# Performance work log

Measured on AMD Instinct MI355X. Metric: run time of the kernel, lower is better.

## Reference

```python
import jax, jax.numpy as jnp
import numpy as np

N, E, F_IN, H, MH, C, G = 100000, 3200000, 128, 32, 64, 10, 64

def _seg_sum(data, ids, num):
    return jax.ops.segment_sum(data, ids, num_segments=num)

def gcn_conv(x, row, col, ew, W, b, n):
    # PyG GCNConv: linear first, then self-loops + symmetric edge-weight norm + scatter-add
    h = x @ W  # [N, H]
    loop = jnp.arange(n)
    r = jnp.concatenate([row, loop])
    c = jnp.concatenate([col, loop])
    w = jnp.concatenate([ew, jnp.ones((n,), dtype=ew.dtype)])
    deg = _seg_sum(w, c, n)
    dinv = jnp.where(deg > 0, jax.lax.rsqrt(deg), 0.0)
    norm = dinv[r] * w * dinv[c]  # [E+N]
    out = _seg_sum(norm[:, None] * h[r], c, n)  # scatter to targets
    return out + b

def setup_inputs():
    key = jax.random.key(0)
    ks = jax.random.split(key, 16)
    inp = {
        "x": jax.random.normal(ks[0], (N, F_IN), dtype=jnp.float32),
        "edge_index": jax.random.randint(ks[1], (2, E), 0, N, dtype=jnp.int64),
        "edge_weight": jax.random.uniform(ks[2], (E,), dtype=jnp.float32),
        "batch": jnp.sort(jax.random.randint(ks[3], (N,), 0, G, dtype=jnp.int64)),
    }
    def lin(k, i, o):
        s = 1.0 / np.sqrt(i)
        k1, k2 = jax.random.split(k)
        return (jax.random.uniform(k1, (i, o), minval=-s, maxval=s, dtype=jnp.float32),
                jax.random.uniform(k2, (o,), minval=-s, maxval=s, dtype=jnp.float32))
    inp["W1"], inp["b1"] = lin(ks[4], F_IN, H)
    inp["W2"], inp["b2"] = lin(ks[5], H, H)
    inp["W3"], inp["b3"] = lin(ks[6], H, H)
    inp["Wm0"], inp["bm0"] = lin(ks[7], H, MH)
    inp["Wm1"], inp["bm1"] = lin(ks[8], MH, MH)
    inp["Wout"], inp["bout"] = lin(ks[9], MH, C)
    return inp

def reference(x, edge_index, edge_weight, batch, W1, b1, W2, b2, W3, b3, Wm0, bm0, Wm1, bm1, Wout, bout):
    row, col = edge_index[0], edge_index[1]
    h = jax.nn.relu(gcn_conv(x, row, col, edge_weight, W1, b1, N))
    h = jax.nn.relu(gcn_conv(h, row, col, edge_weight, W2, b2, N))
    h = gcn_conv(h, row, col, edge_weight, W3, b3, N)
    # global mean pool over graphs
    sums = _seg_sum(h, batch, G)
    counts = _seg_sum(jnp.ones((N,), dtype=h.dtype), batch, G)
    g = sums / jnp.maximum(counts, 1.0)[:, None]
    # dropout p=0.5 is identity at inference (training=False)
    g = jax.nn.relu(g @ Wm0 + bm0)
    g = jax.nn.relu(g @ Wm1 + bm1)
    return g @ Wout + bout
```

## Files before the change

kernel.cpp:

```cpp
#include <hip/hip_runtime.h>

#define NN 100000
#define NE 3200000
#define FIN 128
#define HID 32
#define MH  64
#define NC  10
#define NG  64
#define NBKT 782
#define NBLK 512
#define EPB  (NE / NBLK)
#define SCANL (NBKT * NBLK)
#define SRCMASK 0x1FFFF
#define BCAP 5120

typedef float floatx2 __attribute__((ext_vector_type(2)));

__global__ __launch_bounds__(1024)
void hist_bkt(const int* __restrict__ ei, int* __restrict__ cnt2) {
    __shared__ int h[NBKT];
    int tid = threadIdx.x, blk = blockIdx.x;
    for (int b = tid; b < NBKT; b += 1024) h[b] = 0;
    __syncthreads();
    int base = blk * EPB;
    for (int i = tid; i < EPB; i += 1024)
        atomicAdd(&h[ei[NE + base + i] >> 7], 1);
    __syncthreads();
    for (int b = tid; b < NBKT; b += 1024) cnt2[b * NBLK + blk] = h[b];
}

__global__ void scan_block(const int* __restrict__ in, int* __restrict__ out,
                           int* __restrict__ bsum, int n) {
    __shared__ int lds[256];
    int tid = threadIdx.x;
    int base = blockIdx.x * 1024 + tid * 4;
    int v0 = 0, v1 = 0, v2 = 0, v3 = 0;
    if (base + 0 < n) v0 = in[base + 0];
    if (base + 1 < n) v1 = in[base + 1];
    if (base + 2 < n) v2 = in[base + 2];
    if (base + 3 < n) v3 = in[base + 3];
    int s = v0 + v1 + v2 + v3;
    lds[tid] = s;
    __syncthreads();
    for (int off = 1; off < 256; off <<= 1) {
        int val = (tid >= off) ? lds[tid - off] : 0;
        __syncthreads();
        lds[tid] += val;
        __syncthreads();
    }
    int excl = lds[tid] - s;
    if (tid == 255) bsum[blockIdx.x] = lds[255];
    if (base + 0 < n) out[base + 0] = excl;
    if (base + 1 < n) out[base + 1] = excl + v0;
    if (base + 2 < n) out[base + 2] = excl + v0 + v1;
    if (base + 3 < n) out[base + 3] = excl + v0 + v1 + v2;
}

__global__ void scan_top(int* __restrict__ bsum, int nb, float* __restrict__ sc) {
    int lane = threadIdx.x;
    for (int i = lane; i < NG * HID + NG; i += 64) sc[i] = 0.0f;
    int carry = 0;
    for (int base = 0; base < nb; base += 64) {
        int i = base + lane;
        int orig = (i < nb) ? bsum[i] : 0;
        int v = orig;
#pragma unroll
        for (int off = 1; off < 64; off <<= 1) {
            int t = __shfl_up(v, off, 64);
            if (lane >= off) v += t;
        }
        if (i < nb) bsum[i] = carry + v - orig;
        carry += __shfl(v, 63, 64);
    }
}

__global__ void scan_add(int* __restrict__ data, const int* __restrict__ bsum, int n) {
    int i = blockIdx.x * 256 + threadIdx.x;
    if (i < n) data[i] += bsum[i >> 10];
}

__global__ __launch_bounds__(1024)
void scatter_bkt(const int* __restrict__ ei, const float* __restrict__ ew,
                 const int* __restrict__ cnt2, const int* __restrict__ scanned,
                 int2* __restrict__ tre) {
    __shared__ int2 pay[EPB];
    __shared__ int scur[NBKT];
    __shared__ int hexc[NBKT];
    __shared__ int gbase[NBKT];
    int tid = threadIdx.x, blk = blockIdx.x;
    int myh = 0;
    if (tid < NBKT) {
        myh = cnt2[tid * NBLK + blk];
        gbase[tid] = scanned[tid * NBLK + blk];
        scur[tid] = myh;
    }
    __syncthreads();
    for (int off = 1; off < NBKT; off <<= 1) {
        int v = (tid < NBKT && tid >= off) ? scur[tid - off] : 0;
        __syncthreads();
        if (tid < NBKT) scur[tid] += v;
        __syncthreads();
    }
    if (tid < NBKT) { int ex = scur[tid] - myh; hexc[tid] = ex; scur[tid] = ex; }
    __syncthreads();
    int base = blk * EPB;
    for (int i = tid; i < EPB; i += 1024) {
        int e = base + i;
        int c = ei[NE + e];
        int r = ei[e];
        unsigned int wb = __float_as_uint(ew[e]);
        int b = c >> 7;
        int j = atomicAdd(&scur[b], 1);
        pay[j] = make_int2(r | ((c & 127) << 17) | ((b & 0xFF) << 24),
                           (int)((wb & ~3u) | ((unsigned)b >> 8)));
    }
    __syncthreads();
    for (int j = tid; j < EPB; j += 1024) {
        int2 q = pay[j];
        int b = (int)((((unsigned)q.y & 3u) << 8) | (((unsigned)q.x >> 24) & 0xFFu));
        int pos = gbase[b] + (j - hexc[b]);
        tre[pos] = make_int2(q.x & 0x00FFFFFF, q.y & ~3);
    }
}

__global__ __launch_bounds__(512)
void sort_k(const int2* __restrict__ tre, const int* __restrict__ scanned,
            unsigned int* __restrict__ srn4, int* __restrict__ rowptr,
            float* __restrict__ dinv) {
    __shared__ int2 ed[BCAP];
    __shared__ int h[128];
    __shared__ float dw[128];
    __shared__ int cur[128];
    int b = blockIdx.x, tid = threadIdx.x;
    int base = scanned[b * NBLK];
    int end = (b == NBKT - 1) ? NE : scanned[(b + 1) * NBLK];
    int n = end - base;
    bool staged = (n <= BCAP);
    if (tid < 128) { h[tid] = 0; dw[tid] = 0.f; }
    __syncthreads();
    for (int i = tid; i < n; i += 512) {
        int2 q = tre[base + i];
        if (staged) ed[i] = q;
        int key = (q.x >> 17) & 127;
        atomicAdd(&h[key], 1);
        atomicAdd(&dw[key], __int_as_float(q.y));
    }
    __syncthreads();
    if (tid < 64) {
        int lane = tid;
        int carry = 0;
#pragma unroll
        for (int c = 0; c < 2; ++c) {
            int idx = c * 64 + lane;
            int hv = h[idx];
            int v = hv;
#pragma unroll
            for (int off = 1; off < 64; off <<= 1) {
                int t = __shfl_up(v, off, 64);
                if (lane >= off) v += t;
            }
            cur[idx] = base + carry + v - hv;
            int node = b * 128 + idx;
            if (node < NN) {
                rowptr[node] = base + carry + v;
                dinv[node] = rsqrtf(1.0f + dw[idx]);
            }
            carry += __shfl(v, 63, 64);
        }
    }
    __syncthreads();
    for (int i = tid; i < n; i += 512) {
        int2 q = staged ? ed[i] : tre[base + i];
        int key = (q.x >> 17) & 127;
        int pos = atomicAdd(&cur[key], 1);
        unsigned int wb = (unsigned)q.y;
        wb += 0x7FFFu + ((wb >> 16) & 1u);
        srn4[pos] = (unsigned)(q.x & SRCMASK) | (((wb >> 16) & 0x7FFFu) << 17);
    }
}

template <int IN_DIM, bool RELU_IN>
__global__ __launch_bounds__(256)
void linear_k(const float* __restrict__ in, const float* __restrict__ W,
              const float* __restrict__ dinv, unsigned int* __restrict__ tmp8) {
    constexpr int J4 = IN_DIM / 4;
    constexpr int XSS = J4 + 1;
    __shared__ float4 xs[64 * XSS];
    __shared__ float4 wp[IN_DIM * 8];
    int tid = threadIdx.x;
    for (int idx = tid; idx < IN_DIM * 8; idx += 256) {
        int j = idx >> 3, kg = idx & 7;
        const float* wr = W + j * 32 + kg * 4;
        wp[idx] = make_float4(wr[0], wr[1], wr[2], wr[3]);
    }
    int rbase = blockIdx.x * 64;
    const float4* in4 = (const float4*)in;
    for (int idx = tid; idx < 64 * J4; idx += 256) {
        int row = idx / J4, j4 = idx % J4;
        int grow = rbase + row;
        float4 v = (grow < NN) ? in4[(size_t)grow * J4 + j4]
                               : make_float4(0.f, 0.f, 0.f, 0.f);
        if (RELU_IN) {
            v.x = fmaxf(v.x, 0.f); v.y = fmaxf(v.y, 0.f);
            v.z = fmaxf(v.z, 0.f); v.w = fmaxf(v.w, 0.f);
        }
        xs[row * XSS + j4] = v;
    }
    __syncthreads();
    int kg = tid & 7;
    int rp = tid >> 3;
    int r0 = rbase + 2 * rp;
    if (r0 >= NN) return;
    const float4* x0 = &xs[(2 * rp) * XSS];
    const float4* x1 = &xs[(2 * rp + 1) * XSS];
    float a00 = 0, a01 = 0, a02 = 0, a03 = 0;
    float a10 = 0, a11 = 0, a12 = 0, a13 = 0;
#pragma unroll
    for (int j4 = 0; j4 < J4; ++j4) {
        float4 v0 = x0[j4], v1 = x1[j4];
        const float4* wj = &wp[j4 * 4 * 8 + kg];
        float4 w0 = wj[0], w1 = wj[8], w2 = wj[16], w3 = wj[24];
#define LSTEP(VX0, VX1, W4) \
        a00 = fmaf(VX0, W4.x, a00); a01 = fmaf(VX0, W4.y, a01); \
        a02 = fmaf(VX0, W4.z, a02); a03 = fmaf(VX0, W4.w, a03); \
        a10 = fmaf(VX1, W4.x, a10); a11 = fmaf(VX1, W4.y, a11); \
        a12 = fmaf(VX1, W4.z, a12); a13 = fmaf(VX1, W4.w, a13);
        LSTEP(v0.x, v1.x, w0)
        LSTEP(v0.y, v1.y, w1)
        LSTEP(v0.z, v1.z, w2)
        LSTEP(v0.w, v1.w, w3)
#undef LSTEP
    }
    float d0 = dinv[r0], d1 = dinv[r0 + 1];
    a00 *= d0; a01 *= d0; a02 *= d0; a03 *= d0;
    a10 *= d1; a11 *= d1; a12 *= d1; a13 *= d1;
    int q0 = __builtin_amdgcn_cvt_pk_fp8_f32(a00, a01, 0, false);
    q0 = __builtin_amdgcn_cvt_pk_fp8_f32(a02, a03, q0, true);
    int q1 = __builtin_amdgcn_cvt_pk_fp8_f32(a10, a11, 0, false);
    q1 = __builtin_amdgcn_cvt_pk_fp8_f32(a12, a13, q1, true);
    tmp8[r0 * 8 + kg] = (unsigned int)q0;
    tmp8[(r0 + 1) * 8 + kg] = (unsigned int)q1;
}

__device__ __forceinline__ float4 agg_core(const unsigned int* __restrict__ srn4,
                                           const int* __restrict__ rowptr,
                                           const unsigned int* __restrict__ tmp8,
                                           int wid, int g, int q) {
    unsigned int qb = (unsigned int)q * 4u;
    const char* t8 = (const char*)tmp8;
    int end = rowptr[wid];
    int start = (wid == 0) ? 0 : rowptr[wid - 1];
    floatx2 a01 = {0.f, 0.f}, a23 = {0.f, 0.f};
    floatx2 c01 = {0.f, 0.f}, c23 = {0.f, 0.f};
    int e = start + g;
    for (; e + 24 < end; e += 32) {
        unsigned int p0 = srn4[e];
        unsigned int p1 = srn4[e + 8];
        unsigned int p2 = srn4[e + 16];
        unsigned int p3 = srn4[e + 24];
        unsigned int u0 = *(const unsigned int*)(t8 + (((p0 & SRCMASK) << 5) | qb));
        unsigned int u1 = *(const unsigned int*)(t8 + (((p1 & SRCMASK) << 5) | qb));
        unsigned int u2 = *(const unsigned int*)(t8 + (((p2 & SRCMASK) << 5) | qb));
        unsigned int u3 = *(const unsigned int*)(t8 + (((p3 & SRCMASK) << 5) | qb));
        float w0 = __uint_as_float((p0 >> 1) & 0x7FFF0000u);
        float w1 = __uint_as_float((p1 >> 1) & 0x7FFF0000u);
        float w2 = __uint_as_float((p2 >> 1) & 0x7FFF0000u);
        float w3 = __uint_as_float((p3 >> 1) & 0x7FFF0000u);
        floatx2 lo, hi;
        lo = __builtin_amdgcn_cvt_pk_f32_fp8(u0, false);
        hi = __builtin_amdgcn_cvt_pk_f32_fp8(u0, true);
        a01 += lo * w0; a23 += hi * w0;
        lo = __builtin_amdgcn_cvt_pk_f32_fp8(u1, false);
        hi = __builtin_amdgcn_cvt_pk_f32_fp8(u1, true);
        c01 += lo * w1; c23 += hi * w1;
        lo = __builtin_amdgcn_cvt_pk_f32_fp8(u2, false);
        hi = __builtin_amdgcn_cvt_pk_f32_fp8(u2, true);
        a01 += lo * w2; a23 += hi * w2;
        lo = __builtin_amdgcn_cvt_pk_f32_fp8(u3, false);
        hi = __builtin_amdgcn_cvt_pk_f32_fp8(u3, true);
        c01 += lo * w3; c23 += hi * w3;
    }
    for (; e < end; e += 8) {
        unsigned int p = srn4[e];
        unsigned int u = *(const unsigned int*)(t8 + (((p & SRCMASK) << 5) | qb));
        float w = __uint_as_float((p >> 1) & 0x7FFF0000u);
        floatx2 lo = __builtin_amdgcn_cvt_pk_f32_fp8(u, false);
        floatx2 hi = __builtin_amdgcn_cvt_pk_f32_fp8(u, true);
        a01 += lo * w; a23 += hi * w;
    }
    a01 += c01; a23 += c23;
    float a0 = a01.x, a1 = a01.y, a2 = a23.x, a3 = a23.y;
    a0 += __shfl_xor(a0, 8, 64);  a1 += __shfl_xor(a1, 8, 64);
    a2 += __shfl_xor(a2, 8, 64);  a3 += __shfl_xor(a3, 8, 64);
    a0 += __shfl_xor(a0, 16, 64); a1 += __shfl_xor(a1, 16, 64);
    a2 += __shfl_xor(a2, 16, 64); a3 += __shfl_xor(a3, 16, 64);
    a0 += __shfl_xor(a0, 32, 64); a1 += __shfl_xor(a1, 32, 64);
    a2 += __shfl_xor(a2, 32, 64); a3 += __shfl_xor(a3, 32, 64);
    return make_float4(a0, a1, a2, a3);
}

__global__ __launch_bounds__(256)
void aggregate(const unsigned int* __restrict__ srn4,
               const int* __restrict__ rowptr,
               const float* __restrict__ dinv,
               const float* __restrict__ bias,
               const unsigned int* __restrict__ tmp8,
               float* __restrict__ h) {
    int tid = threadIdx.x;
    int wid = (blockIdx.x * 256 + tid) >> 6;
    if (wid >= NN) return;
    int lane = tid & 63;
    int g = lane >> 3, q = lane & 7;
    float4 a = agg_core(srn4, rowptr, tmp8, wid, g, q);
    if (g == 0) {
        float d = dinv[wid];
        unsigned int sv = tmp8[(size_t)wid * 8 + q];
        floatx2 slo = __builtin_amdgcn_cvt_pk_f32_fp8(sv, false);
        floatx2 shi = __builtin_amdgcn_cvt_pk_f32_fp8(sv, true);
        float4 bq = ((const float4*)bias)[q];
        float4 o;
        o.x = bq.x + d * (slo.x + a.x);
        o.y = bq.y + d * (slo.y + a.y);
        o.z = bq.z + d * (shi.x + a.z);
        o.w = bq.w + d * (shi.y + a.w);
        ((float4*)(h + (size_t)wid * HID))[q] = o;
    }
}

__global__ __launch_bounds__(256)
void agg_lin(const unsigned int* __restrict__ srn4,
             const int* __restrict__ rowptr,
             const float* __restrict__ dinv,
             const float* __restrict__ bias,
             const float* __restrict__ Wn,
             const unsigned int* __restrict__ tmp8,
             unsigned int* __restrict__ tmp8_out) {
    __shared__ float hrow[4][HID];
    int tid = threadIdx.x;
    int wid = (blockIdx.x * 256 + tid) >> 6;
    int wv = tid >> 6;
    int lane = tid & 63;
    int g = lane >> 3, q = lane & 7;
    float4 a = agg_core(srn4, rowptr, tmp8, wid, g, q);
    float d = dinv[wid];
    if (g == 0) {
        unsigned int sv = tmp8[(size_t)wid * 8 + q];
        floatx2 slo = __builtin_amdgcn_cvt_pk_f32_fp8(sv, false);
        floatx2 shi = __builtin_amdgcn_cvt_pk_f32_fp8(sv, true);
        float4 bq = ((const float4*)bias)[q];
        float4 o;
        o.x = fmaxf(bq.x + d * (slo.x + a.x), 0.f);
        o.y = fmaxf(bq.y + d * (slo.y + a.y), 0.f);
        o.z = fmaxf(bq.z + d * (shi.x + a.z), 0.f);
        o.w = fmaxf(bq.w + d * (shi.y + a.w), 0.f);
        *((float4*)&hrow[wv][4 * q]) = o;
    }
    int j = lane & 31, half = lane >> 5;
    const float4* h4 = (const float4*)&hrow[wv][half * 16];
    float4 h0 = h4[0], h1 = h4[1], h2 = h4[2], h3 = h4[3];
    float hh[16];
    *((float4*)&hh[0]) = h0; *((float4*)&hh[4]) = h1;
    *((float4*)&hh[8]) = h2; *((float4*)&hh[12]) = h3;
    const float* wc = Wn + half * 16 * 32 + j;
    float y = 0.f;
#pragma unroll
    for (int k = 0; k < 16; ++k)
        y = fmaf(hh[k], wc[k * 32], y);
    y += __shfl_xor(y, 32, 64);
    y *= d;
    float y1 = __shfl_down(y, 1, 64);
    float y2 = __shfl_down(y, 2, 64);
    float y3 = __shfl_down(y, 3, 64);
    if (half == 0 && (j & 3) == 0) {
        int w0 = __builtin_amdgcn_cvt_pk_fp8_f32(y, y1, 0, false);
        w0 = __builtin_amdgcn_cvt_pk_fp8_f32(y2, y3, w0, true);
        tmp8_out[wid * 8 + (j >> 2)] = (unsigned int)w0;
    }
}

__global__ void pool_k(const float* __restrict__ h, const int* __restrict__ batch,
                       float* __restrict__ sums, float* __restrict__ counts) {
    int t = blockIdx.x * 256 + threadIdx.x;
    int chunk = t >> 5, k = t & 31;
    int n0 = chunk * 32;
    if (n0 >= NN) return;
    int n1 = min(n0 + 32, NN);
    int g = batch[n0];
    float acc = 0.f, cacc = 0.f;
    for (int i = n0; i < n1; ++i) {
        int gi = batch[i];
        if (gi != g) {
            atomicAdd(&sums[g * HID + k], acc);
            if (k == 0) atomicAdd(&counts[g], cacc);
            g = gi; acc = 0.f; cacc = 0.f;
        }
        acc += h[(size_t)i * HID + k];
        cacc += 1.f;
    }
    atomicAdd(&sums[g * HID + k], acc);
    if (k == 0) atomicAdd(&counts[g], cacc);
}

__global__ __launch_bounds__(64)
void mlp_k(const float* __restrict__ sums, const float* __restrict__ counts,
           const float* __restrict__ Wm0, const float* __restrict__ bm0,
           const float* __restrict__ Wm1, const float* __restrict__ bm1,
           const float* __restrict__ Wout, const float* __restrict__ bout,
           float* __restrict__ out) {
    __shared__ float g0[HID];
    __shared__ float g1[MH];
    __shared__ float g2[MH];
    int g = blockIdx.x;
    int k = threadIdx.x;
    if (k < HID) g0[k] = sums[g * HID + k] / fmaxf(counts[g], 1.0f);
    __syncthreads();
    float acc = bm0[k];
#pragma unroll
    for (int j = 0; j < HID; ++j) acc = fmaf(g0[j], Wm0[j * MH + k], acc);
    g1[k] = fmaxf(acc, 0.f);
    __syncthreads();
    float acc2 = bm1[k];
#pragma unroll
    for (int j = 0; j < MH; ++j) acc2 = fmaf(g1[j], Wm1[j * MH + k], acc2);
    g2[k] = fmaxf(acc2, 0.f);
    __syncthreads();
    if (k < NC) {
        float acc3 = bout[k];
#pragma unroll
        for (int j = 0; j < MH; ++j) acc3 = fmaf(g2[j], Wout[j * NC + k], acc3);
        out[g * NC + k] = acc3;
    }
}

extern "C" void kernel_launch(void* const* d_in, const int* in_sizes, int n_in,
                              void* d_out, int out_size, void* d_ws, size_t ws_size,
                              hipStream_t stream) {
    const float* x    = (const float*)d_in[0];
    const int*   ei   = (const int*)d_in[1];
    const float* ew   = (const float*)d_in[2];
    const int*   batch= (const int*)d_in[3];
    const float* W1   = (const float*)d_in[4];
    const float* b1   = (const float*)d_in[5];
    const float* W2   = (const float*)d_in[6];
    const float* b2   = (const float*)d_in[7];
    const float* W3   = (const float*)d_in[8];
    const float* b3   = (const float*)d_in[9];
    const float* Wm0  = (const float*)d_in[10];
    const float* bm0  = (const float*)d_in[11];
    const float* Wm1  = (const float*)d_in[12];
    const float* bm1  = (const float*)d_in[13];
    const float* Wout = (const float*)d_in[14];
    const float* bout = (const float*)d_in[15];
    float* out = (float*)d_out;

    char* p = (char*)d_ws;
    unsigned int* srn4 = (unsigned int*)p; p += sizeof(unsigned int) * (size_t)NE;
    char*  S   = p;                      p += 12 * (size_t)NE;
    int2*  tre = (int2*)S;
    int*   cnt2    = (int*)(S + sizeof(int2) * (size_t)NE);
    int*   scanned = cnt2 + SCANL;
    unsigned int* tmp8  = (unsigned int*)S;
    unsigned int* tmp8b = tmp8 + (size_t)NN * 8;
    float* hA  = (float*)(S + 2 * (size_t)NN * HID);
    int*   bsum    = (int*)p;            p += sizeof(int) * 512;
    float* dinv    = (float*)p;          p += sizeof(float) * NN;
    int*   rowptr  = (int*)p;            p += sizeof(int) * NN;
    float* sums    = (float*)p;          p += sizeof(float) * NG * HID;
    float* counts  = (float*)p;

    dim3 blk(256);
    const int NB_SCAN = (SCANL + 1023) / 1024;
    const int NB_LIN = (NN + 63) / 64;

    hist_bkt<<<NBLK, 1024, 0, stream>>>(ei, cnt2);
    scan_block<<<NB_SCAN, blk, 0, stream>>>(cnt2, scanned, bsum, SCANL);
    scan_top<<<1, 64, 0, stream>>>(bsum, NB_SCAN, sums);
    scan_add<<<(SCANL + 255) / 256, blk, 0, stream>>>(scanned, bsum, SCANL);
    scatter_bkt<<<NBLK, 1024, 0, stream>>>(ei, ew, cnt2, scanned, tre);
    sort_k<<<NBKT, 512, 0, stream>>>(tre, scanned, srn4, rowptr, dinv);

    linear_k<FIN, false><<<NB_LIN, blk, 0, stream>>>(x, W1, dinv, tmp8);
    agg_lin<<<25000, blk, 0, stream>>>(srn4, rowptr, dinv, b1, W2, tmp8, tmp8b);
    agg_lin<<<25000, blk, 0, stream>>>(srn4, rowptr, dinv, b2, W3, tmp8b, tmp8);
    aggregate<<<25000, blk, 0, stream>>>(srn4, rowptr, dinv, b3, tmp8, hA);

    pool_k<<<391, blk, 0, stream>>>(hA, batch, sums, counts);
    mlp_k<<<NG, 64, 0, stream>>>(sums, counts, Wm0, bm0, Wm1, bm1, Wout, bout, out);
}
```

Measured before the change: 398.8 us.

## Aggregate one node per half-wavefront with 8-byte fp8 gathers per lane

The three aggregation kernels now give each node 32 lanes instead of a full 64-lane wavefront. Each lane loads 8 fp8 features (uint2) instead of 4, and 8 edge slots are processed in parallel. The cross-lane reduction shrinks to three shuffle stages, and the fused linear step in agg_lin runs a full 32-wide dot product per lane with no half-split shuffle, which halves the grid. The aim is to raise useful lanes per gather and cut reduction and launch overhead. The cost is more registers per lane and more accumulator work per thread.

Result: faster. 370.7 us (-7.0%).

```diff
diff --git a/kernel.cpp b/kernel.cpp
--- a/kernel.cpp
+++ b/kernel.cpp
@@ -242,61 +242,78 @@
     tmp8[(r0 + 1) * 8 + kg] = (unsigned int)q1;
 }
 
-__device__ __forceinline__ float4 agg_core(const unsigned int* __restrict__ srn4,
-                                           const int* __restrict__ rowptr,
-                                           const unsigned int* __restrict__ tmp8,
-                                           int wid, int g, int q) {
-    unsigned int qb = (unsigned int)q * 4u;
+struct AccR { floatx2 r0, r1, r2, r3; };
+
+__device__ __forceinline__ AccR agg_core(const unsigned int* __restrict__ srn4,
+                                         const int* __restrict__ rowptr,
+                                         const unsigned int* __restrict__ tmp8,
+                                         int nid, int s, unsigned int cb) {
     const char* t8 = (const char*)tmp8;
-    int end = rowptr[wid];
-    int start = (wid == 0) ? 0 : rowptr[wid - 1];
-    floatx2 a01 = {0.f, 0.f}, a23 = {0.f, 0.f};
-    floatx2 c01 = {0.f, 0.f}, c23 = {0.f, 0.f};
-    int e = start + g;
+    int end = rowptr[nid];
+    int start = (nid == 0) ? 0 : rowptr[nid - 1];
+    floatx2 a0 = {0.f, 0.f}, a1 = {0.f, 0.f}, a2 = {0.f, 0.f}, a3 = {0.f, 0.f};
+    floatx2 b0 = {0.f, 0.f}, b1 = {0.f, 0.f}, b2 = {0.f, 0.f}, b3 = {0.f, 0.f};
+    int e = start + s;
     for (; e + 24 < end; e += 32) {
         unsigned int p0 = srn4[e];
         unsigned int p1 = srn4[e + 8];
         unsigned int p2 = srn4[e + 16];
         unsigned int p3 = srn4[e + 24];
-        unsigned int u0 = *(const unsigned int*)(t8 + (((p0 & SRCMASK) << 5) | qb));
-        unsigned int u1 = *(const unsigned int*)(t8 + (((p1 & SRCMASK) << 5) | qb));
-        unsigned int u2 = *(const unsigned int*)(t8 + (((p2 & SRCMASK) << 5) | qb));
-        unsigned int u3 = *(const unsigned int*)(t8 + (((p3 & SRCMASK) << 5) | qb));
+        uint2 u0 = *(const uint2*)(t8 + (((p0 & SRCMASK) << 5) | cb));
+        uint2 u1 = *(const uint2*)(t8 + (((p1 & SRCMASK) << 5) | cb));
+        uint2 u2 = *(const uint2*)(t8 + (((p2 & SRCMASK) << 5) | cb));
+        uint2 u3 = *(const uint2*)(t8 + (((p3 & SRCMASK) << 5) | cb));
         float w0 = __uint_as_float((p0 >> 1) & 0x7FFF0000u);
         float w1 = __uint_as_float((p1 >> 1) & 0x7FFF0000u);
         float w2 = __uint_as_float((p2 >> 1) & 0x7FFF0000u);
         float w3 = __uint_as_float((p3 >> 1) & 0x7FFF0000u);
         floatx2 lo, hi;
-        lo = __builtin_amdgcn_cvt_pk_f32_fp8(u0, false);
-        hi = __builtin_amdgcn_cvt_pk_f32_fp8(u0, true);
-        a01 += lo * w0; a23 += hi * w0;
-        lo = __builtin_amdgcn_cvt_pk_f32_fp8(u1, false);
-        hi = __builtin_amdgcn_cvt_pk_f32_fp8(u1, true);
-        c01 += lo * w1; c23 += hi * w1;
-        lo = __builtin_amdgcn_cvt_pk_f32_fp8(u2, false);
-        hi = __builtin_amdgcn_cvt_pk_f32_fp8(u2, true);
-        a01 += lo * w2; a23 += hi * w2;
-        lo = __builtin_amdgcn_cvt_pk_f32_fp8(u3, false);
-        hi = __builtin_amdgcn_cvt_pk_f32_fp8(u3, true);
-        c01 += lo * w3; c23 += hi * w3;
+        lo = __builtin_amdgcn_cvt_pk_f32_fp8(u0.x, false);
+        hi = __builtin_amdgcn_cvt_pk_f32_fp8(u0.x, true);
+        a0 += lo * w0; a1 += hi * w0;
+        lo = __builtin_amdgcn_cvt_pk_f32_fp8(u0.y, false);
+        hi = __builtin_amdgcn_cvt_pk_f32_fp8(u0.y, true);
+        a2 += lo * w0; a3 += hi * w0;
+        lo = __builtin_amdgcn_cvt_pk_f32_fp8(u1.x, false);
+        hi = __builtin_amdgcn_cvt_pk_f32_fp8(u1.x, true);
+        b0 += lo * w1; b1 += hi * w1;
+        lo = __builtin_amdgcn_cvt_pk_f32_fp8(u1.y, false);
+        hi = __builtin_amdgcn_cvt_pk_f32_fp8(u1.y, true);
+        b2 += lo * w1; b3 += hi * w1;
+        lo = __builtin_amdgcn_cvt_pk_f32_fp8(u2.x, false);
+        hi = __builtin_amdgcn_cvt_pk_f32_fp8(u2.x, true);
+        a0 += lo * w2; a1 += hi * w2;
+        lo = __builtin_amdgcn_cvt_pk_f32_fp8(u2.y, false);
+        hi = __builtin_amdgcn_cvt_pk_f32_fp8(u2.y, true);
+        a2 += lo * w2; a3 += hi * w2;
+        lo = __builtin_amdgcn_cvt_pk_f32_fp8(u3.x, false);
+        hi = __builtin_amdgcn_cvt_pk_f32_fp8(u3.x, true);
+        b0 += lo * w3; b1 += hi * w3;
+        lo = __builtin_amdgcn_cvt_pk_f32_fp8(u3.y, false);
+        hi = __builtin_amdgcn_cvt_pk_f32_fp8(u3.y, true);
+        b2 += lo * w3; b3 += hi * w3;
     }
     for (; e < end; e += 8) {
         unsigned int p = srn4[e];
-        unsigned int u = *(const unsigned int*)(t8 + (((p & SRCMASK) << 5) | qb));
+        uint2 u = *(const uint2*)(t8 + (((p & SRCMASK) << 5) | cb));
         float w = __uint_as_float((p >> 1) & 0x7FFF0000u);
-        floatx2 lo = __builtin_amdgcn_cvt_pk_f32_fp8(u, false);
-        floatx2 hi = __builtin_amdgcn_cvt_pk_f32_fp8(u, true);
-        a01 += lo * w; a23 += hi * w;
-    }
-    a01 += c01; a23 += c23;
-    float a0 = a01.x, a1 = a01.y, a2 = a23.x, a3 = a23.y;
-    a0 += __shfl_xor(a0, 8, 64);  a1 += __shfl_xor(a1, 8, 64);
-    a2 += __shfl_xor(a2, 8, 64);  a3 += __shfl_xor(a3, 8, 64);
-    a0 += __shfl_xor(a0, 16, 64); a1 += __shfl_xor(a1, 16, 64);
-    a2 += __shfl_xor(a2, 16, 64); a3 += __shfl_xor(a3, 16, 64);
-    a0 += __shfl_xor(a0, 32, 64); a1 += __shfl_xor(a1, 32, 64);
-    a2 += __shfl_xor(a2, 32, 64); a3 += __shfl_xor(a3, 32, 64);
-    return make_float4(a0, a1, a2, a3);
+        floatx2 lo = __builtin_amdgcn_cvt_pk_f32_fp8(u.x, false);
+        floatx2 hi = __builtin_amdgcn_cvt_pk_f32_fp8(u.x, true);
+        a0 += lo * w; a1 += hi * w;
+        lo = __builtin_amdgcn_cvt_pk_f32_fp8(u.y, false);
+        hi = __builtin_amdgcn_cvt_pk_f32_fp8(u.y, true);
+        a2 += lo * w; a3 += hi * w;
+    }
+    a0 += b0; a1 += b1; a2 += b2; a3 += b3;
+#pragma unroll
+    for (int m = 4; m <= 16; m <<= 1) {
+        a0.x += __shfl_xor(a0.x, m, 64); a0.y += __shfl_xor(a0.y, m, 64);
+        a1.x += __shfl_xor(a1.x, m, 64); a1.y += __shfl_xor(a1.y, m, 64);
+        a2.x += __shfl_xor(a2.x, m, 64); a2.y += __shfl_xor(a2.y, m, 64);
+        a3.x += __shfl_xor(a3.x, m, 64); a3.y += __shfl_xor(a3.y, m, 64);
+    }
+    AccR r; r.r0 = a0; r.r1 = a1; r.r2 = a2; r.r3 = a3;
+    return r;
 }
 
 __global__ __launch_bounds__(256)
@@ -307,23 +324,33 @@
                const unsigned int* __restrict__ tmp8,
                float* __restrict__ h) {
     int tid = threadIdx.x;
-    int wid = (blockIdx.x * 256 + tid) >> 6;
-    if (wid >= NN) return;
-    int lane = tid & 63;
-    int g = lane >> 3, q = lane & 7;
-    float4 a = agg_core(srn4, rowptr, tmp8, wid, g, q);
-    if (g == 0) {
-        float d = dinv[wid];
-        unsigned int sv = tmp8[(size_t)wid * 8 + q];
-        floatx2 slo = __builtin_amdgcn_cvt_pk_f32_fp8(sv, false);
-        floatx2 shi = __builtin_amdgcn_cvt_pk_f32_fp8(sv, true);
-        float4 bq = ((const float4*)bias)[q];
-        float4 o;
-        o.x = bq.x + d * (slo.x + a.x);
-        o.y = bq.y + d * (slo.y + a.y);
-        o.z = bq.z + d * (shi.x + a.z);
-        o.w = bq.w + d * (shi.y + a.w);
-        ((float4*)(h + (size_t)wid * HID))[q] = o;
+    int nid = (blockIdx.x * 256 + tid) >> 5;
+    int hl = tid & 31;
+    int c = hl & 3, s = hl >> 2;
+    unsigned int cb = (unsigned int)c * 8u;
+    AccR A = agg_core(srn4, rowptr, tmp8, nid, s, cb);
+    if (hl < 4) {
+        float d = dinv[nid];
+        const char* t8 = (const char*)tmp8;
+        uint2 sv = *(const uint2*)(t8 + ((unsigned int)nid << 5) + cb);
+        floatx2 s0 = __builtin_amdgcn_cvt_pk_f32_fp8(sv.x, false);
+        floatx2 s1 = __builtin_amdgcn_cvt_pk_f32_fp8(sv.x, true);
+        floatx2 s2 = __builtin_amdgcn_cvt_pk_f32_fp8(sv.y, false);
+        floatx2 s3 = __builtin_amdgcn_cvt_pk_f32_fp8(sv.y, true);
+        const float4* b4 = (const float4*)bias;
+        float4 bq0 = b4[2 * c], bq1 = b4[2 * c + 1];
+        float4 o0, o1;
+        o0.x = bq0.x + d * (s0.x + A.r0.x);
+        o0.y = bq0.y + d * (s0.y + A.r0.y);
+        o0.z = bq0.z + d * (s1.x + A.r1.x);
+        o0.w = bq0.w + d * (s1.y + A.r1.y);
+        o1.x = bq1.x + d * (s2.x + A.r2.x);
+        o1.y = bq1.y + d * (s2.y + A.r2.y);
+        o1.z = bq1.z + d * (s3.x + A.r3.x);
+        o1.w = bq1.w + d * (s3.y + A.r3.y);
+        float4* hp = (float4*)(h + (size_t)nid * HID);
+        hp[2 * c] = o0;
+        hp[2 * c + 1] = o1;
     }
 }
 
@@ -335,46 +362,61 @@
              const float* __restrict__ Wn,
              const unsigned int* __restrict__ tmp8,
              unsigned int* __restrict__ tmp8_out) {
-    __shared__ float hrow[4][HID];
+    __shared__ float hrow[4][2][HID];
     int tid = threadIdx.x;
-    int wid = (blockIdx.x * 256 + tid) >> 6;
+    int nid = (blockIdx.x * 256 + tid) >> 5;
     int wv = tid >> 6;
-    int lane = tid & 63;
-    int g = lane >> 3, q = lane & 7;
-    float4 a = agg_core(srn4, rowptr, tmp8, wid, g, q);
-    float d = dinv[wid];
-    if (g == 0) {
-        unsigned int sv = tmp8[(size_t)wid * 8 + q];
-        floatx2 slo = __builtin_amdgcn_cvt_pk_f32_fp8(sv, false);
-        floatx2 shi = __builtin_amdgcn_cvt_pk_f32_fp8(sv, true);
-        float4 bq = ((const float4*)bias)[q];
-        float4 o;
-        o.x = fmaxf(bq.x + d * (slo.x + a.x), 0.f);
-        o.y = fmaxf(bq.y + d * (slo.y + a.y), 0.f);
-        o.z = fmaxf(bq.z + d * (shi.x + a.z), 0.f);
-        o.w = fmaxf(bq.w + d * (shi.y + a.w), 0.f);
-        *((float4*)&hrow[wv][4 * q]) = o;
-    }
-    int j = lane & 31, half = lane >> 5;
-    const float4* h4 = (const float4*)&hrow[wv][half * 16];
+    int half = (tid >> 5) & 1;
+    int hl = tid & 31;
+    int c = hl & 3, s = hl >> 2;
+    unsigned int cb = (unsigned int)c * 8u;
+    AccR A = agg_core(srn4, rowptr, tmp8, nid, s, cb);
+    float d = dinv[nid];
+    if (hl < 4) {
+        const char* t8 = (const char*)tmp8;
+        uint2 sv = *(const uint2*)(t8 + ((unsigned int)nid << 5) + cb);
+        floatx2 s0 = __builtin_amdgcn_cvt_pk_f32_fp8(sv.x, false);
+        floatx2 s1 = __builtin_amdgcn_cvt_pk_f32_fp8(sv.x, true);
+        floatx2 s2 = __builtin_amdgcn_cvt_pk_f32_fp8(sv.y, false);
+        floatx2 s3 = __builtin_amdgcn_cvt_pk_f32_fp8(sv.y, true);
+        const float4* b4 = (const float4*)bias;
+        float4 bq0 = b4[2 * c], bq1 = b4[2 * c + 1];
+        float4 o0, o1;
+        o0.x = fmaxf(bq0.x + d * (s0.x + A.r0.x), 0.f);
+        o0.y = fmaxf(bq0.y + d * (s0.y + A.r0.y), 0.f);
+        o0.z = fmaxf(bq0.z + d * (s1.x + A.r1.x), 0.f);
+        o0.w = fmaxf(bq0.w + d * (s1.y + A.r1.y), 0.f);
+        o1.x = fmaxf(bq1.x + d * (s2.x + A.r2.x), 0.f);
+        o1.y = fmaxf(bq1.y + d * (s2.y + A.r2.y), 0.f);
+        o1.z = fmaxf(bq1.z + d * (s3.x + A.r3.x), 0.f);
+        o1.w = fmaxf(bq1.w + d * (s3.y + A.r3.y), 0.f);
+        float4* hp = (float4*)&hrow[wv][half][0];
+        hp[2 * c] = o0;
+        hp[2 * c + 1] = o1;
+    }
+    int j = hl;
+    const float* hr = hrow[wv][half];
+    const float4* h4 = (const float4*)hr;
     float4 h0 = h4[0], h1 = h4[1], h2 = h4[2], h3 = h4[3];
-    float hh[16];
-    *((float4*)&hh[0]) = h0; *((float4*)&hh[4]) = h1;
-    *((float4*)&hh[8]) = h2; *((float4*)&hh[12]) = h3;
-    const float* wc = Wn + half * 16 * 32 + j;
+    float4 h4v = h4[4], h5 = h4[5], h6 = h4[6], h7 = h4[7];
+    float hh[32];
+    *((float4*)&hh[0]) = h0;  *((float4*)&hh[4]) = h1;
+    *((float4*)&hh[8]) = h2;  *((float4*)&hh[12]) = h3;
+    *((float4*)&hh[16]) = h4v; *((float4*)&hh[20]) = h5;
+    *((float4*)&hh[24]) = h6;  *((float4*)&hh[28]) = h7;
+    const float* wc = Wn + j;
     float y = 0.f;
 #pragma unroll
-    for (int k = 0; k < 16; ++k)
+    for (int k = 0; k < 32; ++k)
         y = fmaf(hh[k], wc[k * 32], y);
-    y += __shfl_xor(y, 32, 64);
     y *= d;
     float y1 = __shfl_down(y, 1, 64);
     float y2 = __shfl_down(y, 2, 64);
     float y3 = __shfl_down(y, 3, 64);
-    if (half == 0 && (j & 3) == 0) {
+    if ((hl & 3) == 0) {
         int w0 = __builtin_amdgcn_cvt_pk_fp8_f32(y, y1, 0, false);
         w0 = __builtin_amdgcn_cvt_pk_fp8_f32(y2, y3, w0, true);
-        tmp8_out[wid * 8 + (j >> 2)] = (unsigned int)w0;
+        tmp8_out[nid * 8 + (hl >> 2)] = (unsigned int)w0;
     }
 }
 
@@ -471,6 +513,7 @@
     dim3 blk(256);
     const int NB_SCAN = (SCANL + 1023) / 1024;
     const int NB_LIN = (NN + 63) / 64;
+    const int NB_AGG = 12500;
 
     hist_bkt<<<NBLK, 1024, 0, stream>>>(ei, cnt2);
     scan_block<<<NB_SCAN, blk, 0, stream>>>(cnt2, scanned, bsum, SCANL);
@@ -480,9 +523,9 @@
     sort_k<<<NBKT, 512, 0, stream>>>(tre, scanned, srn4, rowptr, dinv);
 
     linear_k<FIN, false><<<NB_LIN, blk, 0, stream>>>(x, W1, dinv, tmp8);
-    agg_lin<<<25000, blk, 0, stream>>>(srn4, rowptr, dinv, b1, W2, tmp8, tmp8b);
-    agg_lin<<<25000, blk, 0, stream>>>(srn4, rowptr, dinv, b2, W3, tmp8b, tmp8);
-    aggregate<<<25000, blk, 0, stream>>>(srn4, rowptr, dinv, b3, tmp8, hA);
+    agg_lin<<<NB_AGG, blk, 0, stream>>>(srn4, rowptr, dinv, b1, W2, tmp8, tmp8b);
+    agg_lin<<<NB_AGG, blk, 0, stream>>>(srn4, rowptr, dinv, b2, W3, tmp8b, tmp8);
+    aggregate<<<NB_AGG, blk, 0, stream>>>(srn4, rowptr, dinv, b3, tmp8, hA);
 
     pool_k<<<391, blk, 0, stream>>>(hA, batch, sums, counts);
     mlp_k<<<NG, 64, 0, stream>>>(sums, counts, Wm0, bm0, Wm1, bm1, Wout, bout, out);
```

## Aggregate four nodes per wavefront with 16-byte fp8 gathers per lane

Applied to the files above, without the earlier changes.

Changes the aggregation kernels to map 16 lanes per destination node instead of 64. Each lane handles 16 fp8 features through a uint4 gather, so 8 edge slots times 2 column halves cover a node's 32 features. In agg_lin, the next-layer weight matrix is staged transposed in shared memory, and the matrix-vector product is done per node by 16 lanes. The intent is fewer, wider gather loads and less shuffle-reduction overhead per node, at the cost of more registers for accumulators and more load imbalance within a wavefront across nodes of different degree.

Result: faster. 372.5 us (-6.6%).

```diff
diff --git a/kernel.cpp b/kernel.cpp
--- a/kernel.cpp
+++ b/kernel.cpp
@@ -242,62 +242,117 @@
     tmp8[(r0 + 1) * 8 + kg] = (unsigned int)q1;
 }
 
-__device__ __forceinline__ float4 agg_core(const unsigned int* __restrict__ srn4,
-                                           const int* __restrict__ rowptr,
-                                           const unsigned int* __restrict__ tmp8,
-                                           int wid, int g, int q) {
-    unsigned int qb = (unsigned int)q * 4u;
+struct AccR { floatx2 r0, r1, r2, r3, r4, r5, r6, r7; };
+
+#define ACC8(A0,A1,A2,A3,A4,A5,A6,A7, U, W) { \
+    floatx2 lo_, hi_; \
+    lo_ = __builtin_amdgcn_cvt_pk_f32_fp8(U.x, false); \
+    hi_ = __builtin_amdgcn_cvt_pk_f32_fp8(U.x, true); \
+    A0 += lo_ * W; A1 += hi_ * W; \
+    lo_ = __builtin_amdgcn_cvt_pk_f32_fp8(U.y, false); \
+    hi_ = __builtin_amdgcn_cvt_pk_f32_fp8(U.y, true); \
+    A2 += lo_ * W; A3 += hi_ * W; \
+    lo_ = __builtin_amdgcn_cvt_pk_f32_fp8(U.z, false); \
+    hi_ = __builtin_amdgcn_cvt_pk_f32_fp8(U.z, true); \
+    A4 += lo_ * W; A5 += hi_ * W; \
+    lo_ = __builtin_amdgcn_cvt_pk_f32_fp8(U.w, false); \
+    hi_ = __builtin_amdgcn_cvt_pk_f32_fp8(U.w, true); \
+    A6 += lo_ * W; A7 += hi_ * W; }
+
+__device__ __forceinline__ AccR agg_core(const unsigned int* __restrict__ srn4,
+                                         const int* __restrict__ rowptr,
+                                         const unsigned int* __restrict__ tmp8,
+                                         int nid, int s, unsigned int cb) {
     const char* t8 = (const char*)tmp8;
-    int end = rowptr[wid];
-    int start = (wid == 0) ? 0 : rowptr[wid - 1];
-    floatx2 a01 = {0.f, 0.f}, a23 = {0.f, 0.f};
-    floatx2 c01 = {0.f, 0.f}, c23 = {0.f, 0.f};
-    int e = start + g;
+    int end = rowptr[nid];
+    int start = (nid == 0) ? 0 : rowptr[nid - 1];
+    floatx2 a0 = {0.f,0.f}, a1 = {0.f,0.f}, a2 = {0.f,0.f}, a3 = {0.f,0.f};
+    floatx2 a4 = {0.f,0.f}, a5 = {0.f,0.f}, a6 = {0.f,0.f}, a7 = {0.f,0.f};
+    floatx2 b0 = {0.f,0.f}, b1 = {0.f,0.f}, b2 = {0.f,0.f}, b3 = {0.f,0.f};
+    floatx2 b4 = {0.f,0.f}, b5 = {0.f,0.f}, b6 = {0.f,0.f}, b7 = {0.f,0.f};
+    int e = start + s;
     for (; e + 24 < end; e += 32) {
         unsigned int p0 = srn4[e];
         unsigned int p1 = srn4[e + 8];
         unsigned int p2 = srn4[e + 16];
         unsigned int p3 = srn4[e + 24];
-        unsigned int u0 = *(const unsigned int*)(t8 + (((p0 & SRCMASK) << 5) | qb));
-        unsigned int u1 = *(const unsigned int*)(t8 + (((p1 & SRCMASK) << 5) | qb));
-        unsigned int u2 = *(const unsigned int*)(t8 + (((p2 & SRCMASK) << 5) | qb));
-        unsigned int u3 = *(const unsigned int*)(t8 + (((p3 & SRCMASK) << 5) | qb));
+        uint4 u0 = *(const uint4*)(t8 + (((p0 & SRCMASK) << 5) | cb));
+        uint4 u1 = *(const uint4*)(t8 + (((p1 & SRCMASK) << 5) | cb));
+        uint4 u2 = *(const uint4*)(t8 + (((p2 & SRCMASK) << 5) | cb));
+        uint4 u3 = *(const uint4*)(t8 + (((p3 & SRCMASK) << 5) | cb));
         float w0 = __uint_as_float((p0 >> 1) & 0x7FFF0000u);
         float w1 = __uint_as_float((p1 >> 1) & 0x7FFF0000u);
         float w2 = __uint_as_float((p2 >> 1) & 0x7FFF0000u);
         float w3 = __uint_as_float((p3 >> 1) & 0x7FFF0000u);
-        floatx2 lo, hi;
-        lo = __builtin_amdgcn_cvt_pk_f32_fp8(u0, false);
-        hi = __builtin_amdgcn_cvt_pk_f32_fp8(u0, true);
-        a01 += lo * w0; a23 += hi * w0;
-        lo = __builtin_amdgcn_cvt_pk_f32_fp8(u1, false);
-        hi = __builtin_amdgcn_cvt_pk_f32_fp8(u1, true);
-        c01 += lo * w1; c23 += hi * w1;
-        lo = __builtin_amdgcn_cvt_pk_f32_fp8(u2, false);
-        hi = __builtin_amdgcn_cvt_pk_f32_fp8(u2, true);
-        a01 += lo * w2; a23 += hi * w2;
-        lo = __builtin_amdgcn_cvt_pk_f32_fp8(u3, false);
-        hi = __builtin_amdgcn_cvt_pk_f32_fp8(u3, true);
-        c01 += lo * w3; c23 += hi * w3;
+        ACC8(a0,a1,a2,a3,a4,a5,a6,a7, u0, w0)
+        ACC8(b0,b1,b2,b3,b4,b5,b6,b7, u1, w1)
+        ACC8(a0,a1,a2,a3,a4,a5,a6,a7, u2, w2)
+        ACC8(b0,b1,b2,b3,b4,b5,b6,b7, u3, w3)
     }
     for (; e < end; e += 8) {
         unsigned int p = srn4[e];
-        unsigned int u = *(const unsigned int*)(t8 + (((p & SRCMASK) << 5) | qb));
+        uint4 u = *(const uint4*)(t8 + (((p & SRCMASK) << 5) | cb));
         float w = __uint_as_float((p >> 1) & 0x7FFF0000u);
-        floatx2 lo = __builtin_amdgcn_cvt_pk_f32_fp8(u, false);
-        floatx2 hi = __builtin_amdgcn_cvt_pk_f32_fp8(u, true);
-        a01 += lo * w; a23 += hi * w;
-    }
-    a01 += c01; a23 += c23;
-    float a0 = a01.x, a1 = a01.y, a2 = a23.x, a3 = a23.y;
-    a0 += __shfl_xor(a0, 8, 64);  a1 += __shfl_xor(a1, 8, 64);
-    a2 += __shfl_xor(a2, 8, 64);  a3 += __shfl_xor(a3, 8, 64);
-    a0 += __shfl_xor(a0, 16, 64); a1 += __shfl_xor(a1, 16, 64);
-    a2 += __shfl_xor(a2, 16, 64); a3 += __shfl_xor(a3, 16, 64);
-    a0 += __shfl_xor(a0, 32, 64); a1 += __shfl_xor(a1, 32, 64);
-    a2 += __shfl_xor(a2, 32, 64); a3 += __shfl_xor(a3, 32, 64);
-    return make_float4(a0, a1, a2, a3);
-}
+        ACC8(a0,a1,a2,a3,a4,a5,a6,a7, u, w)
+    }
+    a0 += b0; a1 += b1; a2 += b2; a3 += b3;
+    a4 += b4; a5 += b5; a6 += b6; a7 += b7;
+#define REDM(M) { \
+    a0.x += __shfl_xor(a0.x, M, 64); a0.y += __shfl_xor(a0.y, M, 64); \
+    a1.x += __shfl_xor(a1.x, M, 64); a1.y += __shfl_xor(a1.y, M, 64); \
+    a2.x += __shfl_xor(a2.x, M, 64); a2.y += __shfl_xor(a2.y, M, 64); \
+    a3.x += __shfl_xor(a3.x, M, 64); a3.y += __shfl_xor(a3.y, M, 64); \
+    a4.x += __shfl_xor(a4.x, M, 64); a4.y += __shfl_xor(a4.y, M, 64); \
+    a5.x += __shfl_xor(a5.x, M, 64); a5.y += __shfl_xor(a5.y, M, 64); \
+    a6.x += __shfl_xor(a6.x, M, 64); a6.y += __shfl_xor(a6.y, M, 64); \
+    a7.x += __shfl_xor(a7.x, M, 64); a7.y += __shfl_xor(a7.y, M, 64); }
+    REDM(2) REDM(4) REDM(8)
+#undef REDM
+    AccR r;
+    r.r0 = a0; r.r1 = a1; r.r2 = a2; r.r3 = a3;
+    r.r4 = a4; r.r5 = a5; r.r6 = a6; r.r7 = a7;
+    return r;
+}
+
+#define EPILOGUE16(O0,O1,O2,O3, NID, CB, D, BIAS, A, RELU) { \
+    const char* t8_ = (const char*)tmp8; \
+    uint4 sv_ = *(const uint4*)(t8_ + (((unsigned)(NID)) << 5) + (CB)); \
+    floatx2 s0_ = __builtin_amdgcn_cvt_pk_f32_fp8(sv_.x, false); \
+    floatx2 s1_ = __builtin_amdgcn_cvt_pk_f32_fp8(sv_.x, true); \
+    floatx2 s2_ = __builtin_amdgcn_cvt_pk_f32_fp8(sv_.y, false); \
+    floatx2 s3_ = __builtin_amdgcn_cvt_pk_f32_fp8(sv_.y, true); \
+    floatx2 s4_ = __builtin_amdgcn_cvt_pk_f32_fp8(sv_.z, false); \
+    floatx2 s5_ = __builtin_amdgcn_cvt_pk_f32_fp8(sv_.z, true); \
+    floatx2 s6_ = __builtin_amdgcn_cvt_pk_f32_fp8(sv_.w, false); \
+    floatx2 s7_ = __builtin_amdgcn_cvt_pk_f32_fp8(sv_.w, true); \
+    const float4* bp_ = (const float4*)(BIAS) + 4 * c; \
+    float4 bq0_ = bp_[0], bq1_ = bp_[1], bq2_ = bp_[2], bq3_ = bp_[3]; \
+    O0.x = bq0_.x + (D) * (s0_.x + A.r0.x); \
+    O0.y = bq0_.y + (D) * (s0_.y + A.r0.y); \
+    O0.z = bq0_.z + (D) * (s1_.x + A.r1.x); \
+    O0.w = bq0_.w + (D) * (s1_.y + A.r1.y); \
+    O1.x = bq1_.x + (D) * (s2_.x + A.r2.x); \
+    O1.y = bq1_.y + (D) * (s2_.y + A.r2.y); \
+    O1.z = bq1_.z + (D) * (s3_.x + A.r3.x); \
+    O1.w = bq1_.w + (D) * (s3_.y + A.r3.y); \
+    O2.x = bq2_.x + (D) * (s4_.x + A.r4.x); \
+    O2.y = bq2_.y + (D) * (s4_.y + A.r4.y); \
+    O2.z = bq2_.z + (D) * (s5_.x + A.r5.x); \
+    O2.w = bq2_.w + (D) * (s5_.y + A.r5.y); \
+    O3.x = bq3_.x + (D) * (s6_.x + A.r6.x); \
+    O3.y = bq3_.y + (D) * (s6_.y + A.r6.y); \
+    O3.z = bq3_.z + (D) * (s7_.x + A.r7.x); \
+    O3.w = bq3_.w + (D) * (s7_.y + A.r7.y); \
+    if (RELU) { \
+        O0.x = fmaxf(O0.x, 0.f); O0.y = fmaxf(O0.y, 0.f); \
+        O0.z = fmaxf(O0.z, 0.f); O0.w = fmaxf(O0.w, 0.f); \
+        O1.x = fmaxf(O1.x, 0.f); O1.y = fmaxf(O1.y, 0.f); \
+        O1.z = fmaxf(O1.z, 0.f); O1.w = fmaxf(O1.w, 0.f); \
+        O2.x = fmaxf(O2.x, 0.f); O2.y = fmaxf(O2.y, 0.f); \
+        O2.z = fmaxf(O2.z, 0.f); O2.w = fmaxf(O2.w, 0.f); \
+        O3.x = fmaxf(O3.x, 0.f); O3.y = fmaxf(O3.y, 0.f); \
+        O3.z = fmaxf(O3.z, 0.f); O3.w = fmaxf(O3.w, 0.f); \
+    } }
 
 __global__ __launch_bounds__(256)
 void aggregate(const unsigned int* __restrict__ srn4,
@@ -307,23 +362,17 @@
                const unsigned int* __restrict__ tmp8,
                float* __restrict__ h) {
     int tid = threadIdx.x;
-    int wid = (blockIdx.x * 256 + tid) >> 6;
-    if (wid >= NN) return;
+    int nid = (blockIdx.x * 256 + tid) >> 4;
     int lane = tid & 63;
-    int g = lane >> 3, q = lane & 7;
-    float4 a = agg_core(srn4, rowptr, tmp8, wid, g, q);
-    if (g == 0) {
-        float d = dinv[wid];
-        unsigned int sv = tmp8[(size_t)wid * 8 + q];
-        floatx2 slo = __builtin_amdgcn_cvt_pk_f32_fp8(sv, false);
-        floatx2 shi = __builtin_amdgcn_cvt_pk_f32_fp8(sv, true);
-        float4 bq = ((const float4*)bias)[q];
-        float4 o;
-        o.x = bq.x + d * (slo.x + a.x);
-        o.y = bq.y + d * (slo.y + a.y);
-        o.z = bq.z + d * (shi.x + a.z);
-        o.w = bq.w + d * (shi.y + a.w);
-        ((float4*)(h + (size_t)wid * HID))[q] = o;
+    int c = lane & 1, s = (lane >> 1) & 7;
+    unsigned int cb = (unsigned int)c * 16u;
+    AccR A = agg_core(srn4, rowptr, tmp8, nid, s, cb);
+    if ((lane & 14) == 0) {
+        float d = dinv[nid];
+        float4 o0, o1, o2, o3;
+        EPILOGUE16(o0, o1, o2, o3, nid, cb, d, bias, A, false)
+        float4* hp = (float4*)(h + (size_t)nid * HID + 16 * c);
+        hp[0] = o0; hp[1] = o1; hp[2] = o2; hp[3] = o3;
     }
 }
 
@@ -335,46 +384,56 @@
              const float* __restrict__ Wn,
              const unsigned int* __restrict__ tmp8,
              unsigned int* __restrict__ tmp8_out) {
-    __shared__ float hrow[4][HID];
+    __shared__ float hrow[4][4][HID];
+    __shared__ float Wt[32][36];
     int tid = threadIdx.x;
-    int wid = (blockIdx.x * 256 + tid) >> 6;
+    for (int idx = tid; idx < 1024; idx += 256)
+        Wt[idx & 31][idx >> 5] = Wn[idx];
+    int nid = (blockIdx.x * 256 + tid) >> 4;
     int wv = tid >> 6;
     int lane = tid & 63;
-    int g = lane >> 3, q = lane & 7;
-    float4 a = agg_core(srn4, rowptr, tmp8, wid, g, q);
-    float d = dinv[wid];
-    if (g == 0) {
-        unsigned int sv = tmp8[(size_t)wid * 8 + q];
-        floatx2 slo = __builtin_amdgcn_cvt_pk_f32_fp8(sv, false);
-        floatx2 shi = __builtin_amdgcn_cvt_pk_f32_fp8(sv, true);
-        float4 bq = ((const float4*)bias)[q];
-        float4 o;
-        o.x = fmaxf(bq.x + d * (slo.x + a.x), 0.f);
-        o.y = fmaxf(bq.y + d * (slo.y + a.y), 0.f);
-        o.z = fmaxf(bq.z + d * (shi.x + a.z), 0.f);
-        o.w = fmaxf(bq.w + d * (shi.y + a.w), 0.f);
-        *((float4*)&hrow[wv][4 * q]) = o;
-    }
-    int j = lane & 31, half = lane >> 5;
-    const float4* h4 = (const float4*)&hrow[wv][half * 16];
-    float4 h0 = h4[0], h1 = h4[1], h2 = h4[2], h3 = h4[3];
-    float hh[16];
-    *((float4*)&hh[0]) = h0; *((float4*)&hh[4]) = h1;
-    *((float4*)&hh[8]) = h2; *((float4*)&hh[12]) = h3;
-    const float* wc = Wn + half * 16 * 32 + j;
-    float y = 0.f;
-#pragma unroll
-    for (int k = 0; k < 16; ++k)
-        y = fmaf(hh[k], wc[k * 32], y);
-    y += __shfl_xor(y, 32, 64);
-    y *= d;
-    float y1 = __shfl_down(y, 1, 64);
-    float y2 = __shfl_down(y, 2, 64);
-    float y3 = __shfl_down(y, 3, 64);
-    if (half == 0 && (j & 3) == 0) {
-        int w0 = __builtin_amdgcn_cvt_pk_fp8_f32(y, y1, 0, false);
-        w0 = __builtin_amdgcn_cvt_pk_fp8_f32(y2, y3, w0, true);
-        tmp8_out[wid * 8 + (j >> 2)] = (unsigned int)w0;
+    int n = (lane >> 4) & 3;
+    int c = lane & 1, s = (lane >> 1) & 7;
+    unsigned int cb = (unsigned int)c * 16u;
+    __syncthreads();
+    AccR A = agg_core(srn4, rowptr, tmp8, nid, s, cb);
+    float d = dinv[nid];
+    if ((lane & 14) == 0) {
+        float4 o0, o1, o2, o3;
+        EPILOGUE16(o0, o1, o2, o3, nid, cb, d, bias, A, true)
+        float4* hp = (float4*)&hrow[wv][n][16 * c];
+        hp[0] = o0; hp[1] = o1; hp[2] = o2; hp[3] = o3;
+    }
+    int j0 = lane & 15;
+    const float4* hb = (const float4*)&hrow[wv][n][0];
+    float4 h0 = hb[0], h1 = hb[1], h2 = hb[2], h3 = hb[3];
+    float4 h4 = hb[4], h5 = hb[5], h6 = hb[6], h7 = hb[7];
+    const float4* w0p = (const float4*)&Wt[j0][0];
+    const float4* w1p = (const float4*)&Wt[j0 + 16][0];
+    float y0 = 0.f, y1 = 0.f;
+#define MVSTEP(K, HV) { float4 wa_ = w0p[K]; float4 wb_ = w1p[K]; \
+    y0 = fmaf(HV.x, wa_.x, y0); y0 = fmaf(HV.y, wa_.y, y0); \
+    y0 = fmaf(HV.z, wa_.z, y0); y0 = fmaf(HV.w, wa_.w, y0); \
+    y1 = fmaf(HV.x, wb_.x, y1); y1 = fmaf(HV.y, wb_.y, y1); \
+    y1 = fmaf(HV.z, wb_.z, y1); y1 = fmaf(HV.w, wb_.w, y1); }
+    MVSTEP(0, h0) MVSTEP(1, h1) MVSTEP(2, h2) MVSTEP(3, h3)
+    MVSTEP(4, h4) MVSTEP(5, h5) MVSTEP(6, h6) MVSTEP(7, h7)
+#undef MVSTEP
+    y0 *= d; y1 *= d;
+    float p1 = __shfl_down(y0, 1, 64);
+    float p2 = __shfl_down(y0, 2, 64);
+    float p3 = __shfl_down(y0, 3, 64);
+    float q1 = __shfl_down(y1, 1, 64);
+    float q2 = __shfl_down(y1, 2, 64);
+    float q3 = __shfl_down(y1, 3, 64);
+    if ((j0 & 3) == 0) {
+        int t = j0 >> 2;
+        int w0 = __builtin_amdgcn_cvt_pk_fp8_f32(y0, p1, 0, false);
+        w0 = __builtin_amdgcn_cvt_pk_fp8_f32(p2, p3, w0, true);
+        int w1 = __builtin_amdgcn_cvt_pk_fp8_f32(y1, q1, 0, false);
+        w1 = __builtin_amdgcn_cvt_pk_fp8_f32(q2, q3, w1, true);
+        tmp8_out[nid * 8 + t] = (unsigned int)w0;
+        tmp8_out[nid * 8 + 4 + t] = (unsigned int)w1;
     }
 }
 
@@ -471,6 +530,7 @@
     dim3 blk(256);
     const int NB_SCAN = (SCANL + 1023) / 1024;
     const int NB_LIN = (NN + 63) / 64;
+    const int NB_AGG = 6250;
 
     hist_bkt<<<NBLK, 1024, 0, stream>>>(ei, cnt2);
     scan_block<<<NB_SCAN, blk, 0, stream>>>(cnt2, scanned, bsum, SCANL);
@@ -480,9 +540,9 @@
     sort_k<<<NBKT, 512, 0, stream>>>(tre, scanned, srn4, rowptr, dinv);
 
     linear_k<FIN, false><<<NB_LIN, blk, 0, stream>>>(x, W1, dinv, tmp8);
-    agg_lin<<<25000, blk, 0, stream>>>(srn4, rowptr, dinv, b1, W2, tmp8, tmp8b);
-    agg_lin<<<25000, blk, 0, stream>>>(srn4, rowptr, dinv, b2, W3, tmp8b, tmp8);
-    aggregate<<<25000, blk, 0, stream>>>(srn4, rowptr, dinv, b3, tmp8, hA);
+    agg_lin<<<NB_AGG, blk, 0, stream>>>(srn4, rowptr, dinv, b1, W2, tmp8, tmp8b);
+    agg_lin<<<NB_AGG, blk, 0, stream>>>(srn4, rowptr, dinv, b2, W3, tmp8b, tmp8);
+    aggregate<<<NB_AGG, blk, 0, stream>>>(srn4, rowptr, dinv, b3, tmp8, hA);
 
     pool_k<<<391, blk, 0, stream>>>(hA, batch, sums, counts);
     mlp_k<<<NG, 64, 0, stream>>>(sums, counts, Wm0, bm0, Wm1, bm1, Wout, bout, out);
```
